# Kernel tuning notes

Measured on AMD Instinct MI355X. Metric: run time of the kernel, lower is better.

The kernel has to match this reference:

```python
import jax, jax.numpy as jnp
import numpy as np

B, S, D, F = 8, 4096, 512, 4

def setup_inputs() -> dict:
    key = jax.random.key(0)
    k1, k2, k3, k4 = jax.random.split(key, 4)
    return {
        "inputs": jax.random.normal(k1, (B, S, D), dtype=jnp.float32),
        "values": jax.random.normal(k2, (B, S, F * D), dtype=jnp.float32),
        "W_out": jax.random.normal(k3, (2 * D, D), dtype=jnp.float32) * 0.02,
        "w_score": jax.random.normal(k4, (D, 1), dtype=jnp.float32) * 0.02,
        "b_score": jnp.zeros((1,), dtype=jnp.float32),
        "n": F,
    }

def reference(inputs, values, W_out, w_score, b_score, n):
    # inputs: [B,S,D]; values: [B,S,F*D] -> per-position lattice factors [B,S,F,D]
    b, s, d = inputs.shape
    f = values.shape[2] // d
    mem = values.reshape(b, s, f, d)
    # dot-attention of each position's query over its F factor vectors
    scores = jnp.einsum('bsd,bsfd->bsf', inputs, mem)  # [B,S,F]
    valid = jnp.arange(f) < n                          # lattice mask from n
    scores = jnp.where(valid, scores, jnp.float32(-1e9))
    attn = jax.nn.softmax(scores, axis=-1)
    ctx = jnp.einsum('bsf,bsfd->bsd', attn, mem)       # [B,S,D]
    # OpenNMT GlobalAttention (dot): tanh(linear_out([ctx; q])), no bias
    cat = jnp.concatenate([ctx, inputs], axis=-1)      # [B,S,2D]
    attn_h = jnp.tanh(cat @ W_out)                     # [B,S,D]
    # sigmoid context gate from the query
    gate = jax.nn.sigmoid(inputs @ w_score + b_score)  # [B,S,1]
    # dropout is identity in eval; residual add
    return attn_h * gate + inputs
```

## Files before the change

### kernel.cpp

```cpp
#include <hip/hip_runtime.h>
#include <hip/hip_bf16.h>
#include <math.h>

#define BATCH 8
#define SEQ   4096
#define DIM   512
#define FDIM  4
#define M_TOTAL (BATCH*SEQ)
#define K_TOTAL (2*DIM)
#define N_TOTAL DIM

#define PRE_BLOCKS (M_TOTAL/4)
#define WCONV_BLOCKS ((K_TOTAL/64)*(N_TOTAL/64))

#define BM 128
#define BN 128
#define BK 64
#define NKT (K_TOTAL/BK)
#define GEMM_BLOCKS ((M_TOTAL/BM)*(N_TOTAL/BN))

typedef __bf16 bf16x8 __attribute__((ext_vector_type(8)));
typedef float  f32x4  __attribute__((ext_vector_type(4)));

__device__ __forceinline__ void gload_lds16(const void* g, void* l) {
    __builtin_amdgcn_global_load_lds(
        (__attribute__((address_space(1))) void*)(void*)g,
        (__attribute__((address_space(3))) void*)l,
        16, 0, 0);
}

__device__ __forceinline__ float dot4(float4 a, float4 b) {
    return a.x*b.x + a.y*b.y + a.z*b.z + a.w*b.w;
}

__device__ __forceinline__ void store_bf4(__hip_bfloat16* dst, float4 v) {
    __hip_bfloat16 t[4];
    t[0] = __float2bfloat16(v.x); t[1] = __float2bfloat16(v.y);
    t[2] = __float2bfloat16(v.z); t[3] = __float2bfloat16(v.w);
    *reinterpret_cast<uint2*>(dst) = *reinterpret_cast<const uint2*>(t);
}

__device__ __forceinline__ float fast_tanh(float x) {
    float e = __expf(2.f * x);
    return 1.f - 2.f * __builtin_amdgcn_rcpf(e + 1.f);
}

__global__ __launch_bounds__(256)
void pre_kernel(const float* __restrict__ inputs,
                const float* __restrict__ values,
                const float* __restrict__ W,
                const float* __restrict__ w_score,
                const float* __restrict__ b_score,
                const int*   __restrict__ n_ptr,
                __hip_bfloat16* __restrict__ cat,
                float* __restrict__ gate,
                __hip_bfloat16* __restrict__ Wt)
{
    __shared__ float ws[64][65];

    const int tid  = threadIdx.x;

    if (blockIdx.x >= PRE_BLOCKS) {
        const int t  = blockIdx.x - PRE_BLOCKS;
        const int k0 = (t & 15) * 64;
        const int n0 = (t >> 4) * 64;
        #pragma unroll
        for (int i = 0; i < 16; ++i) {
            int e = i * 256 + tid;
            int r = e >> 6, c = e & 63;
            ws[r][c] = W[(size_t)(k0 + r) * N_TOTAL + n0 + c];
        }
        __syncthreads();
        #pragma unroll
        for (int i = 0; i < 16; ++i) {
            int e = i * 256 + tid;
            int nr = e >> 6, kc = e & 63;
            Wt[(size_t)(n0 + nr) * K_TOTAL + k0 + kc] = __float2bfloat16(ws[kc][nr]);
        }
        return;
    }

    const int lane = tid & 63;
    const int wv   = tid >> 6;
    const int p    = blockIdx.x * 4 + wv;

    const float4* qg = (const float4*)(inputs + (size_t)p * DIM);
    float4 qa = qg[lane], qb = qg[lane + 64];

    const float4* vg = (const float4*)(values + (size_t)p * (FDIM*DIM));
    float4 ma[4], mb[4];
    float s[4];
    #pragma unroll
    for (int f = 0; f < 4; ++f) {
        ma[f] = vg[f * 128 + lane];
        mb[f] = vg[f * 128 + lane + 64];
        s[f] = dot4(qa, ma[f]) + dot4(qb, mb[f]);
    }
    const float4* wg = (const float4*)w_score;
    float g = dot4(qa, wg[lane]) + dot4(qb, wg[lane + 64]);

    #pragma unroll
    for (int off = 1; off < 64; off <<= 1) {
        s[0] += __shfl_xor(s[0], off, 64);
        s[1] += __shfl_xor(s[1], off, 64);
        s[2] += __shfl_xor(s[2], off, 64);
        s[3] += __shfl_xor(s[3], off, 64);
        g    += __shfl_xor(g,    off, 64);
    }

    const int nv = *n_ptr;
    #pragma unroll
    for (int f = 0; f < 4; ++f) if (f >= nv) s[f] = -1e9f;
    float mx = fmaxf(fmaxf(s[0], s[1]), fmaxf(s[2], s[3]));
    float e0 = __expf(s[0] - mx), e1 = __expf(s[1] - mx);
    float e2 = __expf(s[2] - mx), e3 = __expf(s[3] - mx);
    float inv = __builtin_amdgcn_rcpf(e0 + e1 + e2 + e3);
    float a[4] = { e0 * inv, e1 * inv, e2 * inv, e3 * inv };

    float4 ca = {0.f, 0.f, 0.f, 0.f}, cb = {0.f, 0.f, 0.f, 0.f};
    #pragma unroll
    for (int f = 0; f < 4; ++f) {
        ca.x += a[f] * ma[f].x; ca.y += a[f] * ma[f].y;
        ca.z += a[f] * ma[f].z; ca.w += a[f] * ma[f].w;
        cb.x += a[f] * mb[f].x; cb.y += a[f] * mb[f].y;
        cb.z += a[f] * mb[f].z; cb.w += a[f] * mb[f].w;
    }

    __hip_bfloat16* cp = cat + (size_t)p * K_TOTAL;
    store_bf4(cp +        4 * lane, ca);
    store_bf4(cp + 256  + 4 * lane, cb);
    store_bf4(cp + 512  + 4 * lane, qa);
    store_bf4(cp + 768  + 4 * lane, qb);

    if (lane == 0) {
        float t = g + b_score[0];
        gate[p] = __builtin_amdgcn_rcpf(1.f + __expf(-t));
    }
}

__global__ __launch_bounds__(256, 4)
void gemm_ep(const __hip_bfloat16* __restrict__ A,
             const __hip_bfloat16* __restrict__ Bt,
             const float* __restrict__ gate,
             float* __restrict__ out)
{
    __shared__ __align__(16) __hip_bfloat16 As[BM * BK];
    __shared__ __align__(16) __hip_bfloat16 Bs[BN * BK];
    __shared__ float gateLds[BM];

    const int tid = threadIdx.x;
    const int bm = blockIdx.x >> 2;
    const int bn = blockIdx.x & 3;

    const int wid  = tid >> 6;
    const int lane = tid & 63;
    const int wr   = wid >> 1;
    const int wc   = wid & 1;
    const int la   = lane & 15;
    const int lb   = lane >> 4;

    const __hip_bfloat16* Ag = A  + (size_t)(bm * BM) * K_TOTAL;
    const __hip_bfloat16* Bg = Bt + (size_t)(bn * BN) * K_TOTAL;

    if (tid < BM) gateLds[tid] = gate[bm * BM + tid];

    f32x4 acc[4][4] = {};

    for (int kt = 0; kt < K_TOTAL; kt += BK) {
        __syncthreads();
        #pragma unroll
        for (int ps = 0; ps < 4; ++ps) {
            int cl  = ps * 256 + tid;
            int row = cl >> 3;
            int c   = cl & 7;
            int sc_ = c ^ (row & 7);
            gload_lds16(Ag + (size_t)row * K_TOTAL + kt + sc_ * 8, As + cl * 8);
            gload_lds16(Bg + (size_t)row * K_TOTAL + kt + sc_ * 8, Bs + cl * 8);
        }
        __syncthreads();

        #pragma unroll
        for (int kk = 0; kk < 2; ++kk) {
            bf16x8 af[4], bfv[4];
            #pragma unroll
            for (int i = 0; i < 4; ++i) {
                int row = wr * 64 + i * 16 + la;
                int cc  = (kk * 4 + lb) ^ (row & 7);
                af[i] = *reinterpret_cast<const bf16x8*>(As + row * BK + cc * 8);
            }
            #pragma unroll
            for (int j = 0; j < 4; ++j) {
                int row = wc * 64 + j * 16 + la;
                int cc  = (kk * 4 + lb) ^ (row & 7);
                bfv[j] = *reinterpret_cast<const bf16x8*>(Bs + row * BK + cc * 8);
            }
            #pragma unroll
            for (int i = 0; i < 4; ++i)
                #pragma unroll
                for (int j = 0; j < 4; ++j)
                    acc[i][j] = __builtin_amdgcn_mfma_f32_16x16x32_bf16(af[i], bfv[j], acc[i][j], 0, 0, 0);
        }
    }

    const int row0 = bm * BM + wr * 64;
    const int col0 = bn * BN + wc * 64;
    #pragma unroll
    for (int i = 0; i < 4; ++i) {
        #pragma unroll
        for (int j = 0; j < 4; ++j) {
            const int col = col0 + j * 16 + la;
            const int rb  = row0 + i * 16 + lb * 4;
            #pragma unroll
            for (int r = 0; r < 4; ++r) {
                const int row = rb + r;
                float q = __bfloat162float(A[(size_t)row * K_TOTAL + 512 + col]);
                float v = fast_tanh(acc[i][j][r]) * gateLds[row - bm * BM] + q;
                out[(size_t)row * DIM + col] = v;
            }
        }
    }
}

extern "C" void kernel_launch(void* const* d_in, const int* in_sizes, int n_in,
                              void* d_out, int out_size, void* d_ws, size_t ws_size,
                              hipStream_t stream) {
    const float* inputs  = (const float*)d_in[0];
    const float* values  = (const float*)d_in[1];
    const float* W_out   = (const float*)d_in[2];
    const float* w_score = (const float*)d_in[3];
    const float* b_score = (const float*)d_in[4];
    const int*   n_ptr   = (const int*)d_in[5];
    float* out = (float*)d_out;

    char* ws = (char*)d_ws;
    __hip_bfloat16* cat  = (__hip_bfloat16*)ws;
    float*          gate = (float*)(ws + (size_t)M_TOTAL * K_TOTAL * 2);
    __hip_bfloat16* Wt   = (__hip_bfloat16*)(ws + (size_t)M_TOTAL * K_TOTAL * 2
                                                + (size_t)M_TOTAL * 4);

    pre_kernel<<<PRE_BLOCKS + WCONV_BLOCKS, 256, 0, stream>>>(
        inputs, values, W_out, w_score, b_score, n_ptr, cat, gate, Wt);
    gemm_ep<<<GEMM_BLOCKS, 256, 0, stream>>>(cat, Wt, gate, out);
}
```

Before: 131.5 us.

## Stop materializing bf16 query copy; convert fp32 inputs inside GEMM loader

The pre-kernel now writes only the bf16 context half instead of a full concatenated [ctx; q] buffer. The GEMM reads fp32 inputs directly for the second half of K and converts them to bf16 in registers before storing to LDS. The epilogue reads the fp32 residual. The change also adds nontemporal loads for values and nontemporal stores for out, and schedules the weight-transpose blocks first. The aim is to cut workspace write and read traffic, at the cost of a synchronous register-staged load path, without async global-to-LDS, for half of the K loop.

```diff
diff --git a/kernel.cpp b/kernel.cpp
--- a/kernel.cpp
+++ b/kernel.cpp
@@ -10,13 +10,12 @@
 #define K_TOTAL (2*DIM)
 #define N_TOTAL DIM
 
+#define WCONV_BLOCKS ((K_TOTAL/64)*(N_TOTAL/64))
 #define PRE_BLOCKS (M_TOTAL/4)
-#define WCONV_BLOCKS ((K_TOTAL/64)*(N_TOTAL/64))
 
 #define BM 128
 #define BN 128
 #define BK 64
-#define NKT (K_TOTAL/BK)
 #define GEMM_BLOCKS ((M_TOTAL/BM)*(N_TOTAL/BN))
 
 typedef __bf16 bf16x8 __attribute__((ext_vector_type(8)));
@@ -29,11 +28,15 @@
         16, 0, 0);
 }
 
-__device__ __forceinline__ float dot4(float4 a, float4 b) {
+__device__ __forceinline__ f32x4 ntload4(const f32x4* p) {
+    return __builtin_nontemporal_load(p);
+}
+
+__device__ __forceinline__ float dot4(f32x4 a, f32x4 b) {
     return a.x*b.x + a.y*b.y + a.z*b.z + a.w*b.w;
 }
 
-__device__ __forceinline__ void store_bf4(__hip_bfloat16* dst, float4 v) {
+__device__ __forceinline__ void store_bf4(__hip_bfloat16* dst, f32x4 v) {
     __hip_bfloat16 t[4];
     t[0] = __float2bfloat16(v.x); t[1] = __float2bfloat16(v.y);
     t[2] = __float2bfloat16(v.z); t[3] = __float2bfloat16(v.w);
@@ -52,16 +55,16 @@
                 const float* __restrict__ w_score,
                 const float* __restrict__ b_score,
                 const int*   __restrict__ n_ptr,
-                __hip_bfloat16* __restrict__ cat,
+                __hip_bfloat16* __restrict__ ctx,
                 float* __restrict__ gate,
                 __hip_bfloat16* __restrict__ Wt)
 {
     __shared__ float ws[64][65];
 
-    const int tid  = threadIdx.x;
-
-    if (blockIdx.x >= PRE_BLOCKS) {
-        const int t  = blockIdx.x - PRE_BLOCKS;
+    const int tid = threadIdx.x;
+
+    if (blockIdx.x < WCONV_BLOCKS) {
+        const int t  = blockIdx.x;
         const int k0 = (t & 15) * 64;
         const int n0 = (t >> 4) * 64;
         #pragma unroll
@@ -82,21 +85,21 @@
 
     const int lane = tid & 63;
     const int wv   = tid >> 6;
-    const int p    = blockIdx.x * 4 + wv;
-
-    const float4* qg = (const float4*)(inputs + (size_t)p * DIM);
-    float4 qa = qg[lane], qb = qg[lane + 64];
-
-    const float4* vg = (const float4*)(values + (size_t)p * (FDIM*DIM));
-    float4 ma[4], mb[4];
+    const int p    = (blockIdx.x - WCONV_BLOCKS) * 4 + wv;
+
+    const f32x4* qg = (const f32x4*)(inputs + (size_t)p * DIM);
+    f32x4 qa = qg[lane], qb = qg[lane + 64];
+
+    const f32x4* vg = (const f32x4*)(values + (size_t)p * (FDIM*DIM));
+    f32x4 ma[4], mb[4];
     float s[4];
     #pragma unroll
     for (int f = 0; f < 4; ++f) {
-        ma[f] = vg[f * 128 + lane];
-        mb[f] = vg[f * 128 + lane + 64];
+        ma[f] = ntload4(vg + f * 128 + lane);
+        mb[f] = ntload4(vg + f * 128 + lane + 64);
         s[f] = dot4(qa, ma[f]) + dot4(qb, mb[f]);
     }
-    const float4* wg = (const float4*)w_score;
+    const f32x4* wg = (const f32x4*)w_score;
     float g = dot4(qa, wg[lane]) + dot4(qb, wg[lane + 64]);
 
     #pragma unroll
@@ -115,33 +118,25 @@
     float e0 = __expf(s[0] - mx), e1 = __expf(s[1] - mx);
     float e2 = __expf(s[2] - mx), e3 = __expf(s[3] - mx);
     float inv = __builtin_amdgcn_rcpf(e0 + e1 + e2 + e3);
-    float a[4] = { e0 * inv, e1 * inv, e2 * inv, e3 * inv };
-
-    float4 ca = {0.f, 0.f, 0.f, 0.f}, cb = {0.f, 0.f, 0.f, 0.f};
-    #pragma unroll
-    for (int f = 0; f < 4; ++f) {
-        ca.x += a[f] * ma[f].x; ca.y += a[f] * ma[f].y;
-        ca.z += a[f] * ma[f].z; ca.w += a[f] * ma[f].w;
-        cb.x += a[f] * mb[f].x; cb.y += a[f] * mb[f].y;
-        cb.z += a[f] * mb[f].z; cb.w += a[f] * mb[f].w;
-    }
-
-    __hip_bfloat16* cp = cat + (size_t)p * K_TOTAL;
-    store_bf4(cp +        4 * lane, ca);
-    store_bf4(cp + 256  + 4 * lane, cb);
-    store_bf4(cp + 512  + 4 * lane, qa);
-    store_bf4(cp + 768  + 4 * lane, qb);
+    float a0 = e0*inv, a1 = e1*inv, a2 = e2*inv, a3 = e3*inv;
+
+    f32x4 ca = ma[0]*a0 + ma[1]*a1 + ma[2]*a2 + ma[3]*a3;
+    f32x4 cb = mb[0]*a0 + mb[1]*a1 + mb[2]*a2 + mb[3]*a3;
+
+    __hip_bfloat16* cp = ctx + (size_t)p * DIM;
+    store_bf4(cp +       4 * lane, ca);
+    store_bf4(cp + 256 + 4 * lane, cb);
 
     if (lane == 0) {
-        float t = g + b_score[0];
-        gate[p] = __builtin_amdgcn_rcpf(1.f + __expf(-t));
+        gate[p] = __builtin_amdgcn_rcpf(1.f + __expf(-(g + b_score[0])));
     }
 }
 
 __global__ __launch_bounds__(256, 4)
-void gemm_ep(const __hip_bfloat16* __restrict__ A,
+void gemm_ep(const __hip_bfloat16* __restrict__ Actx,
              const __hip_bfloat16* __restrict__ Bt,
              const float* __restrict__ gate,
+             const float* __restrict__ inputs,
              float* __restrict__ out)
 {
     __shared__ __align__(16) __hip_bfloat16 As[BM * BK];
@@ -159,7 +154,8 @@
     const int la   = lane & 15;
     const int lb   = lane >> 4;
 
-    const __hip_bfloat16* Ag = A  + (size_t)(bm * BM) * K_TOTAL;
+    const __hip_bfloat16* Ag = Actx + (size_t)(bm * BM) * DIM;
+    const float*          Qg = inputs + (size_t)(bm * BM) * DIM;
     const __hip_bfloat16* Bg = Bt + (size_t)(bn * BN) * K_TOTAL;
 
     if (tid < BM) gateLds[tid] = gate[bm * BM + tid];
@@ -168,14 +164,52 @@
 
     for (int kt = 0; kt < K_TOTAL; kt += BK) {
         __syncthreads();
-        #pragma unroll
-        for (int ps = 0; ps < 4; ++ps) {
-            int cl  = ps * 256 + tid;
-            int row = cl >> 3;
-            int c   = cl & 7;
-            int sc_ = c ^ (row & 7);
-            gload_lds16(Ag + (size_t)row * K_TOTAL + kt + sc_ * 8, As + cl * 8);
-            gload_lds16(Bg + (size_t)row * K_TOTAL + kt + sc_ * 8, Bs + cl * 8);
+        if (kt < 512) {
+            #pragma unroll
+            for (int ps = 0; ps < 4; ++ps) {
+                int cl  = ps * 256 + tid;
+                int row = cl >> 3;
+                int c   = cl & 7;
+                int sc_ = c ^ (row & 7);
+                gload_lds16(Ag + (size_t)row * DIM + kt + sc_ * 8, As + cl * 8);
+                gload_lds16(Bg + (size_t)row * K_TOTAL + kt + sc_ * 8, Bs + cl * 8);
+            }
+        } else {
+            #pragma unroll
+            for (int ps = 0; ps < 4; ++ps) {
+                int cl  = ps * 256 + tid;
+                int row = cl >> 3;
+                int c   = cl & 7;
+                int sc_ = c ^ (row & 7);
+                gload_lds16(Bg + (size_t)row * K_TOTAL + kt + sc_ * 8, Bs + cl * 8);
+            }
+            #pragma unroll
+            for (int bt = 0; bt < 2; ++bt) {
+                f32x4 f[4];
+                int cls[2];
+                #pragma unroll
+                for (int ps = 0; ps < 2; ++ps) {
+                    int cl  = (bt * 2 + ps) * 256 + tid;
+                    int row = cl >> 3;
+                    int c   = cl & 7;
+                    int sc_ = c ^ (row & 7);
+                    const f32x4* src = (const f32x4*)(Qg + (size_t)row * DIM
+                                                      + (kt - 512) + sc_ * 8);
+                    f[ps*2]   = src[0];
+                    f[ps*2+1] = src[1];
+                    cls[ps] = cl;
+                }
+                #pragma unroll
+                for (int ps = 0; ps < 2; ++ps) {
+                    __hip_bfloat16 t[8];
+                    t[0] = __float2bfloat16(f[ps*2].x);   t[1] = __float2bfloat16(f[ps*2].y);
+                    t[2] = __float2bfloat16(f[ps*2].z);   t[3] = __float2bfloat16(f[ps*2].w);
+                    t[4] = __float2bfloat16(f[ps*2+1].x); t[5] = __float2bfloat16(f[ps*2+1].y);
+                    t[6] = __float2bfloat16(f[ps*2+1].z); t[7] = __float2bfloat16(f[ps*2+1].w);
+                    *reinterpret_cast<uint4*>(As + cls[ps] * 8) =
+                        *reinterpret_cast<const uint4*>(t);
+                }
+            }
         }
         __syncthreads();
 
@@ -213,9 +247,9 @@
             #pragma unroll
             for (int r = 0; r < 4; ++r) {
                 const int row = rb + r;
-                float q = __bfloat162float(A[(size_t)row * K_TOTAL + 512 + col]);
+                float q = inputs[(size_t)row * DIM + col];
                 float v = fast_tanh(acc[i][j][r]) * gateLds[row - bm * BM] + q;
-                out[(size_t)row * DIM + col] = v;
+                __builtin_nontemporal_store(v, &out[(size_t)row * DIM + col]);
             }
         }
     }
@@ -233,12 +267,12 @@
     float* out = (float*)d_out;
 
     char* ws = (char*)d_ws;
-    __hip_bfloat16* cat  = (__hip_bfloat16*)ws;
-    float*          gate = (float*)(ws + (size_t)M_TOTAL * K_TOTAL * 2);
-    __hip_bfloat16* Wt   = (__hip_bfloat16*)(ws + (size_t)M_TOTAL * K_TOTAL * 2
+    __hip_bfloat16* ctx  = (__hip_bfloat16*)ws;
+    float*          gate = (float*)(ws + (size_t)M_TOTAL * DIM * 2);
+    __hip_bfloat16* Wt   = (__hip_bfloat16*)(ws + (size_t)M_TOTAL * DIM * 2
                                                 + (size_t)M_TOTAL * 4);
 
-    pre_kernel<<<PRE_BLOCKS + WCONV_BLOCKS, 256, 0, stream>>>(
-        inputs, values, W_out, w_score, b_score, n_ptr, cat, gate, Wt);
-    gemm_ep<<<GEMM_BLOCKS, 256, 0, stream>>>(cat, Wt, gate, out);
-}
+    pre_kernel<<<WCONV_BLOCKS + PRE_BLOCKS, 256, 0, stream>>>(
+        inputs, values, W_out, w_score, b_score, n_ptr, ctx, gate, Wt);
+    gemm_ep<<<GEMM_BLOCKS, 256, 0, stream>>>(ctx, Wt, gate, inputs, out);
+}
```

After: 135.2 us. +2.8%, slower.
